# Optimization experiments

Measured on AMD Instinct MI355X. Metric: run time of the kernel, lower is better.

Reference implementation:

```python
import jax, jax.numpy as jnp
import numpy as np

N_NODES = 100000
N_EDGES = 1600000
D_IN = 128
HID = 128
N_CLS = 10
N_GRAPHS = 128


def _gcn_conv(x, W, b, src, dst, dis, n):
    # x' = W x; out[i] = sum_{(j->i)} d_j^{-1/2} d_i^{-1/2} x'_j ; then + bias
    h = x @ W  # [N, out]
    norm = dis[src] * dis[dst]  # [E_tot]
    msg = h[src] * norm[:, None]  # gather + scale (irregular access)
    out = jax.ops.segment_sum(msg, dst, num_segments=n)  # scatter-add
    return out + b


def setup_inputs() -> dict:
    key = jax.random.key(0)
    ks = jax.random.split(key, 12)
    x = jax.random.normal(ks[0], (N_NODES, D_IN), dtype=jnp.float32)
    edge_index = jax.random.randint(ks[1], (2, N_EDGES), 0, N_NODES, dtype=jnp.int64)
    batch = jnp.sort(jax.random.randint(ks[2], (N_NODES,), 0, N_GRAPHS, dtype=jnp.int64))
    drop_u = jax.random.uniform(ks[3], (N_NODES, D_IN), dtype=jnp.float32)
    s = lambda k, sh, fan: jax.random.normal(k, sh, dtype=jnp.float32) / np.sqrt(fan)
    return {
        "x": x, "edge_index": edge_index, "batch": batch, "num_graphs": N_GRAPHS,
        "drop_u": drop_u,
        "lin1_w": s(ks[4], (D_IN, D_IN), D_IN), "lin1_b": jnp.zeros((D_IN,), jnp.float32),
        "conv1_w": s(ks[5], (D_IN, HID), D_IN), "conv1_b": jnp.zeros((HID,), jnp.float32),
        "conv2_w": s(ks[6], (HID, HID // 2), HID), "conv2_b": jnp.zeros((HID // 2,), jnp.float32),
        "lin2_w": s(ks[7], (HID // 2, N_CLS), HID // 2), "lin2_b": jnp.zeros((N_CLS,), jnp.float32),
    }


def reference(x, edge_index, batch, num_graphs, drop_u,
              lin1_w, lin1_b, conv1_w, conv1_b, conv2_w, conv2_b, lin2_w, lin2_b):
    n = x.shape[0]
    # add self loops (PyG GCNConv default)
    loop = jnp.arange(n, dtype=edge_index.dtype)
    src = jnp.concatenate([edge_index[0], loop])
    dst = jnp.concatenate([edge_index[1], loop])
    deg = jax.ops.segment_sum(jnp.ones_like(dst, dtype=x.dtype), dst, num_segments=n)
    dis = jnp.where(deg > 0, jax.lax.rsqrt(deg), 0.0)  # deg^{-1/2}

    h = x @ lin1_w + lin1_b
    h = _gcn_conv(h, conv1_w, conv1_b, src, dst, dis, n)
    # dropout p=0.5 (training mode in original): keep where u >= 0.5, scale by 2
    h = h * (drop_u >= 0.5).astype(h.dtype) * 2.0
    h = jax.nn.relu(h)
    h = _gcn_conv(h, conv2_w, conv2_b, src, dst, dis, n)
    # global mean pool over graph ids
    sums = jax.ops.segment_sum(h, batch, num_segments=num_graphs)
    cnts = jax.ops.segment_sum(jnp.ones((n,), h.dtype), batch, num_segments=num_graphs)
    pooled = sums / jnp.maximum(cnts, 1.0)[:, None]
    return pooled @ lin2_w + lin2_b
```

## Files before the change

### kernel.cpp

```cpp
#include <hip/hip_runtime.h>
#include <hip/hip_bf16.h>

#define DIN   128
#define HID2  64
#define NCLS  10
#define NGRAPH 128
#define SCAN_CHUNK 1024
#define NBLK 256
#define NBKT_MAX 512
#define CAP 6144

typedef __attribute__((ext_vector_type(8))) short bf16x8;
typedef __attribute__((ext_vector_type(4))) float f32x4;

__device__ __forceinline__ void atomAddF(float* p, float v) {
    unsafeAtomicAdd(p, v);
}

__device__ __forceinline__ unsigned short f2bf(float f) {
    unsigned int u = __float_as_uint(f);
    u += 0x7fffu + ((u >> 16) & 1u);
    return (unsigned short)(u >> 16);
}

__global__ __launch_bounds__(128) void k_w12(const float* __restrict__ lw,
                                             const float* __restrict__ lb,
                                             const float* __restrict__ cw,
                                             float* __restrict__ W12,
                                             float* __restrict__ c1preb) {
    int i = blockIdx.x, j = threadIdx.x;
    const float* arow = (i < 128) ? (lw + i * 128) : lb;
    float acc = 0.f;
#pragma unroll 8
    for (int k = 0; k < 128; ++k) acc += arow[k] * cw[k * 128 + j];
    if (i < 128) W12[i * 128 + j] = acc;
    else         c1preb[j] = acc;
}

__global__ __launch_bounds__(256) void k_bhist(const int* __restrict__ dst,
                                               int* __restrict__ bh, int E, int nbkt,
                                               float* __restrict__ zbuf, int zn) {
    __shared__ int lh[NBKT_MAX];
    if (blockIdx.x == 0)
        for (int i = threadIdx.x; i < zn; i += 256) zbuf[i] = 0.f;
    for (int i = threadIdx.x; i < nbkt; i += 256) lh[i] = 0;
    __syncthreads();
    for (int e = blockIdx.x * 256 + threadIdx.x; e < E; e += NBLK * 256)
        atomicAdd(&lh[__builtin_nontemporal_load(dst + e) >> 8], 1);
    __syncthreads();
    for (int i = threadIdx.x; i < nbkt; i += 256) bh[i * NBLK + blockIdx.x] = lh[i];
}

__global__ __launch_bounds__(256) void k_scan_part(const int* __restrict__ cnt,
                                                   int* __restrict__ part, int n) {
    int base = blockIdx.x * SCAN_CHUNK + threadIdx.x * 4;
    int s = 0;
#pragma unroll
    for (int j = 0; j < 4; ++j) { int i = base + j; if (i < n) s += cnt[i]; }
#pragma unroll
    for (int o = 32; o > 0; o >>= 1) s += __shfl_down(s, o);
    __shared__ int wsum[4];
    if ((threadIdx.x & 63) == 0) wsum[threadIdx.x >> 6] = s;
    __syncthreads();
    if (threadIdx.x == 0) part[blockIdx.x] = wsum[0] + wsum[1] + wsum[2] + wsum[3];
}
__global__ __launch_bounds__(256) void k_scan_mid(int* __restrict__ part,
                                                  int* __restrict__ total_out,
                                                  int B, int n) {
    __shared__ int sh[256];
    int t = threadIdx.x;
    int v = (t < B) ? part[t] : 0;
    sh[t] = v;
    __syncthreads();
    for (int off = 1; off < 256; off <<= 1) {
        int u = (t >= off) ? sh[t - off] : 0;
        __syncthreads();
        sh[t] += u;
        __syncthreads();
    }
    if (t < B) part[t] = sh[t] - v;
    if (t == 255) total_out[n] = sh[255];
}
__global__ __launch_bounds__(256) void k_scan_fin2(const int* cnt,
                                                   const int* __restrict__ part,
                                                   int* out, int n) {
    __shared__ int sh[256];
    int t = threadIdx.x;
    int base = blockIdx.x * SCAN_CHUNK + t * 4;
    int c[4]; int s = 0;
#pragma unroll
    for (int j = 0; j < 4; ++j) { int i = base + j; c[j] = (i < n) ? cnt[i] : 0; s += c[j]; }
    sh[t] = s;
    __syncthreads();
    for (int off = 1; off < 256; off <<= 1) {
        int u = (t >= off) ? sh[t - off] : 0;
        __syncthreads();
        sh[t] += u;
        __syncthreads();
    }
    int excl = part[blockIdx.x] + sh[t] - s;
#pragma unroll
    for (int j = 0; j < 4; ++j) {
        int i = base + j;
        if (i < n) out[i] = excl;
        excl += c[j];
    }
}

__global__ __launch_bounds__(256) void k_partition(const int* __restrict__ src,
                                                   const int* __restrict__ dst,
                                                   const int* __restrict__ bh,
                                                   int* __restrict__ pairs, int E, int nbkt) {
    __shared__ int cur[NBKT_MAX];
    for (int i = threadIdx.x; i < nbkt; i += 256) cur[i] = bh[i * NBLK + blockIdx.x];
    __syncthreads();
    for (int e = blockIdx.x * 256 + threadIdx.x; e < E; e += NBLK * 256) {
        int d = __builtin_nontemporal_load(dst + e);
        int s = __builtin_nontemporal_load(src + e);
        int pos = atomicAdd(&cur[d >> 8], 1);
        pairs[pos] = (s << 8) | (d & 255);
    }
}

__global__ __launch_bounds__(256) void k_csr_local(const int* __restrict__ pairs,
                                                   const int* __restrict__ bh,
                                                   int* __restrict__ row_start,
                                                   float* __restrict__ dis,
                                                   int* __restrict__ col,
                                                   int N) {
    __shared__ int cntL[256], scanL[256], curL[256];
    __shared__ int srcbuf[CAP];
    const int tid = threadIdx.x;
    const int lo = blockIdx.x << 8;
    const int bstart = bh[blockIdx.x * NBLK];
    const int bend = bh[(blockIdx.x + 1) * NBLK];
    const int nE = bend - bstart;

    cntL[tid] = 0;
    __syncthreads();
    for (int e = bstart + tid; e < bend; e += 256)
        atomicAdd(&cntL[pairs[e] & 255], 1);
    __syncthreads();
    const int deg = cntL[tid];
    scanL[tid] = deg;
    __syncthreads();
    for (int off = 1; off < 256; off <<= 1) {
        int u = (tid >= off) ? scanL[tid - off] : 0;
        __syncthreads();
        scanL[tid] += u;
        __syncthreads();
    }
    const int excl = scanL[tid] - deg;
    curL[tid] = excl;
    const int node = lo + tid;
    if (node < N) {
        row_start[node] = bstart + excl;
        dis[node] = rsqrtf((float)(deg + 1));
    } else if (node == N) {
        row_start[N] = bend;
    }
    __syncthreads();
    if (nE <= CAP) {
        for (int e = bstart + tid; e < bend; e += 256) {
            int p = pairs[e];
            int pos = atomicAdd(&curL[p & 255], 1);
            srcbuf[pos] = ((unsigned int)p) >> 8;
        }
        __syncthreads();
        for (int i = tid; i < nE; i += 256)
            col[bstart + i] = srcbuf[i];
    } else {
        for (int e = bstart + tid; e < bend; e += 256) {
            int p = pairs[e];
            int pos = atomicAdd(&curL[p & 255], 1);
            col[bstart + pos] = ((unsigned int)p) >> 8;
        }
    }
}

template <int NCOL>
__global__ __launch_bounds__(256) void k_gemm_mfma(const float* __restrict__ A,
                                                   const float* __restrict__ W,
                                                   const float* __restrict__ bias,
                                                   unsigned short* __restrict__ out, int M) {
    constexpr int KP = 136;
    __shared__ unsigned short As[64 * KP];
    __shared__ unsigned short Wt[NCOL * KP];

    const int tid = threadIdx.x;
    const int row0 = blockIdx.x * 64;

    for (int f = tid; f < 2048; f += 256) {
        int r = f >> 5, c4 = f & 31;
        int gr = row0 + r;
        float4 v = make_float4(0.f, 0.f, 0.f, 0.f);
        if (gr < M) v = *(const float4*)(A + (size_t)gr * 128 + c4 * 4);
        ushort4 b;
        b.x = f2bf(v.x); b.y = f2bf(v.y); b.z = f2bf(v.z); b.w = f2bf(v.w);
        *(ushort4*)(&As[r * KP + c4 * 4]) = b;
    }
    for (int f = tid; f < 32 * NCOL; f += 256) {
        int k = f / (NCOL / 4), n4 = f % (NCOL / 4);
        float4 v = *(const float4*)(W + (size_t)k * NCOL + n4 * 4);
        Wt[(n4 * 4 + 0) * KP + k] = f2bf(v.x);
        Wt[(n4 * 4 + 1) * KP + k] = f2bf(v.y);
        Wt[(n4 * 4 + 2) * KP + k] = f2bf(v.z);
        Wt[(n4 * 4 + 3) * KP + k] = f2bf(v.w);
    }
    __syncthreads();

    const int wave = tid >> 6, lane = tid & 63;
    const int quad = lane >> 4, l16 = lane & 15;
    constexpr int CT = (NCOL == 128) ? 2 : 1;
    const int col0 = wave * 16 * CT;

    f32x4 acc[4][CT];
#pragma unroll
    for (int rt = 0; rt < 4; ++rt)
#pragma unroll
        for (int ct = 0; ct < CT; ++ct) acc[rt][ct] = 0.f;

#pragma unroll
    for (int ks = 0; ks < 4; ++ks) {
        const int kbase = ks * 32 + quad * 8;
        bf16x8 bfr[CT];
#pragma unroll
        for (int ct = 0; ct < CT; ++ct)
            bfr[ct] = *(const bf16x8*)(&Wt[(col0 + ct * 16 + l16) * KP + kbase]);
#pragma unroll
        for (int rt = 0; rt < 4; ++rt) {
            bf16x8 afr = *(const bf16x8*)(&As[(rt * 16 + l16) * KP + kbase]);
#pragma unroll
            for (int ct = 0; ct < CT; ++ct)
                acc[rt][ct] = __builtin_amdgcn_mfma_f32_16x16x32_bf16(afr, bfr[ct], acc[rt][ct], 0, 0, 0);
        }
    }

#pragma unroll
    for (int rt = 0; rt < 4; ++rt)
#pragma unroll
        for (int ct = 0; ct < CT; ++ct) {
            const int c = col0 + ct * 16 + l16;
            const float bv = bias ? bias[c] : 0.f;
#pragma unroll
            for (int reg = 0; reg < 4; ++reg) {
                const int gr = row0 + rt * 16 + quad * 4 + reg;
                if (gr < M) out[(size_t)gr * NCOL + c] = f2bf(acc[rt][ct][reg] + bv);
            }
        }
}

__device__ __forceinline__ unsigned int maskbf2(unsigned int w, float ua, float ub) {
    float a = __uint_as_float(w << 16);
    float b = __uint_as_float(w & 0xffff0000u);
    a = (ua >= 0.5f) ? 2.f * fmaxf(a, 0.f) : 0.f;
    b = (ub >= 0.5f) ? 2.f * fmaxf(b, 0.f) : 0.f;
    return (unsigned int)f2bf(a) | ((unsigned int)f2bf(b) << 16);
}

__global__ __launch_bounds__(256) void k_gemm_bf16in(const unsigned short* __restrict__ A,
                                                     const float* __restrict__ W,
                                                     const float* __restrict__ du,
                                                     unsigned short* __restrict__ out, int M) {
    constexpr int NCOL = 64, KP = 136;
    __shared__ unsigned short As[64 * KP];
    __shared__ unsigned short Wt[NCOL * KP];

    const int tid = threadIdx.x;
    const int row0 = blockIdx.x * 64;

    for (int f = tid; f < 1024; f += 256) {
        int r = f >> 4, c8 = f & 15;
        int gr = row0 + r;
        uint4 b = make_uint4(0u, 0u, 0u, 0u);
        if (gr < M) {
            const uint4 v = *(const uint4*)(A + (size_t)gr * 128 + c8 * 8);
            const float4 u0 = *(const float4*)(du + (size_t)gr * 128 + c8 * 8);
            const float4 u1 = *(const float4*)(du + (size_t)gr * 128 + c8 * 8 + 4);
            b.x = maskbf2(v.x, u0.x, u0.y);
            b.y = maskbf2(v.y, u0.z, u0.w);
            b.z = maskbf2(v.z, u1.x, u1.y);
            b.w = maskbf2(v.w, u1.z, u1.w);
        }
        *(uint4*)(&As[r * KP + c8 * 8]) = b;
    }
    for (int f = tid; f < 32 * NCOL; f += 256) {
        int k = f / (NCOL / 4), n4 = f % (NCOL / 4);
        float4 v = *(const float4*)(W + (size_t)k * NCOL + n4 * 4);
        Wt[(n4 * 4 + 0) * KP + k] = f2bf(v.x);
        Wt[(n4 * 4 + 1) * KP + k] = f2bf(v.y);
        Wt[(n4 * 4 + 2) * KP + k] = f2bf(v.z);
        Wt[(n4 * 4 + 3) * KP + k] = f2bf(v.w);
    }
    __syncthreads();

    const int wave = tid >> 6, lane = tid & 63;
    const int quad = lane >> 4, l16 = lane & 15;
    const int col0 = wave * 16;

    f32x4 acc[4];
#pragma unroll
    for (int rt = 0; rt < 4; ++rt) acc[rt] = 0.f;

#pragma unroll
    for (int ks = 0; ks < 4; ++ks) {
        const int kbase = ks * 32 + quad * 8;
        bf16x8 bfr = *(const bf16x8*)(&Wt[(col0 + l16) * KP + kbase]);
#pragma unroll
        for (int rt = 0; rt < 4; ++rt) {
            bf16x8 afr = *(const bf16x8*)(&As[(rt * 16 + l16) * KP + kbase]);
            acc[rt] = __builtin_amdgcn_mfma_f32_16x16x32_bf16(afr, bfr, acc[rt], 0, 0, 0);
        }
    }

#pragma unroll
    for (int rt = 0; rt < 4; ++rt) {
        const int c = col0 + l16;
#pragma unroll
        for (int reg = 0; reg < 4; ++reg) {
            const int gr = row0 + rt * 16 + quad * 4 + reg;
            if (gr < M) out[(size_t)gr * NCOL + c] = f2bf(acc[rt][reg]);
        }
    }
}

__device__ __forceinline__ void bfacc(uint4 v, float d, float* acc) {
    acc[0] = fmaf(d, __uint_as_float(v.x << 16),        acc[0]);
    acc[1] = fmaf(d, __uint_as_float(v.x & 0xffff0000u), acc[1]);
    acc[2] = fmaf(d, __uint_as_float(v.y << 16),        acc[2]);
    acc[3] = fmaf(d, __uint_as_float(v.y & 0xffff0000u), acc[3]);
    acc[4] = fmaf(d, __uint_as_float(v.z << 16),        acc[4]);
    acc[5] = fmaf(d, __uint_as_float(v.z & 0xffff0000u), acc[5]);
    acc[6] = fmaf(d, __uint_as_float(v.w << 16),        acc[6]);
    acc[7] = fmaf(d, __uint_as_float(v.w & 0xffff0000u), acc[7]);
}

__global__ __launch_bounds__(256) void k_gather_h1(const unsigned short* __restrict__ h,
                                                   const int* __restrict__ row_start,
                                                   const int* __restrict__ col,
                                                   const float* __restrict__ dis,
                                                   const float* __restrict__ bias,
                                                   unsigned short* __restrict__ outb, int n) {
    const int node = (blockIdx.x * 256 + (int)threadIdx.x) >> 4;
    const int l = threadIdx.x & 15;
    if (node >= n) return;
    const int coff = l * 8;

    const float dn = dis[node];
    float acc[8];
    {
        uint4 v = *(const uint4*)(h + (size_t)node * 128 + coff);
#pragma unroll
        for (int q = 0; q < 8; ++q) acc[q] = 0.f;
        bfacc(v, dn, acc);
    }

    const int beg = row_start[node], end = row_start[node + 1];
    int j = beg;
    for (; j + 3 < end; j += 4) {
        const int s0 = col[j], s1 = col[j + 1], s2 = col[j + 2], s3 = col[j + 3];
        const float d0 = dis[s0], d1 = dis[s1], d2 = dis[s2], d3 = dis[s3];
        const uint4 v0 = *(const uint4*)(h + (size_t)s0 * 128 + coff);
        const uint4 v1 = *(const uint4*)(h + (size_t)s1 * 128 + coff);
        const uint4 v2 = *(const uint4*)(h + (size_t)s2 * 128 + coff);
        const uint4 v3 = *(const uint4*)(h + (size_t)s3 * 128 + coff);
        bfacc(v0, d0, acc);
        bfacc(v1, d1, acc);
        bfacc(v2, d2, acc);
        bfacc(v3, d3, acc);
    }
    for (; j < end; ++j) {
        const int s0 = col[j];
        const float d0 = dis[s0];
        const uint4 v0 = *(const uint4*)(h + (size_t)s0 * 128 + coff);
        bfacc(v0, d0, acc);
    }

    const float4 b0 = *(const float4*)(bias + coff);
    const float4 b1 = *(const float4*)(bias + coff + 4);
    const float r0 = fmaf(dn, acc[0], b0.x), r1 = fmaf(dn, acc[1], b0.y);
    const float r2 = fmaf(dn, acc[2], b0.z), r3 = fmaf(dn, acc[3], b0.w);
    const float r4 = fmaf(dn, acc[4], b1.x), r5 = fmaf(dn, acc[5], b1.y);
    const float r6 = fmaf(dn, acc[6], b1.z), r7 = fmaf(dn, acc[7], b1.w);
    uint4 o;
    o.x = (unsigned int)f2bf(r0) | ((unsigned int)f2bf(r1) << 16);
    o.y = (unsigned int)f2bf(r2) | ((unsigned int)f2bf(r3) << 16);
    o.z = (unsigned int)f2bf(r4) | ((unsigned int)f2bf(r5) << 16);
    o.w = (unsigned int)f2bf(r6) | ((unsigned int)f2bf(r7) << 16);
    *(uint4*)(outb + (size_t)node * 128 + coff) = o;
}

__global__ __launch_bounds__(256) void k_gather_pool(const unsigned short* __restrict__ h,
                                                     const int* __restrict__ row_start,
                                                     const int* __restrict__ col,
                                                     const float* __restrict__ dis,
                                                     const float* __restrict__ bias,
                                                     const int* __restrict__ batch,
                                                     float* __restrict__ sums,
                                                     float* __restrict__ cnt, int n) {
    const int node = (blockIdx.x * 256 + (int)threadIdx.x) >> 3;
    const int l = threadIdx.x & 7;
    const int coff = l * 8;
    const bool valid = node < n;

    float r[8];
    int g = 0;
    if (valid) {
        const float dn = dis[node];
        g = batch[node];
        float acc[8];
        {
            uint4 v = *(const uint4*)(h + (size_t)node * 64 + coff);
#pragma unroll
            for (int q = 0; q < 8; ++q) acc[q] = 0.f;
            bfacc(v, dn, acc);
        }
        const int beg = row_start[node], end = row_start[node + 1];
        int j = beg;
        for (; j + 3 < end; j += 4) {
            const int s0 = col[j], s1 = col[j + 1], s2 = col[j + 2], s3 = col[j + 3];
            const float d0 = dis[s0], d1 = dis[s1], d2 = dis[s2], d3 = dis[s3];
            const uint4 v0 = *(const uint4*)(h + (size_t)s0 * 64 + coff);
            const uint4 v1 = *(const uint4*)(h + (size_t)s1 * 64 + coff);
            const uint4 v2 = *(const uint4*)(h + (size_t)s2 * 64 + coff);
            const uint4 v3 = *(const uint4*)(h + (size_t)s3 * 64 + coff);
            bfacc(v0, d0, acc);
            bfacc(v1, d1, acc);
            bfacc(v2, d2, acc);
            bfacc(v3, d3, acc);
        }
        for (; j < end; ++j) {
            const int s0 = col[j];
            const float d0 = dis[s0];
            const uint4 v0 = *(const uint4*)(h + (size_t)s0 * 64 + coff);
            bfacc(v0, d0, acc);
        }
        const float4 b0 = *(const float4*)(bias + coff);
        const float4 b1 = *(const float4*)(bias + coff + 4);
        r[0] = fmaf(dn, acc[0], b0.x); r[1] = fmaf(dn, acc[1], b0.y);
        r[2] = fmaf(dn, acc[2], b0.z); r[3] = fmaf(dn, acc[3], b0.w);
        r[4] = fmaf(dn, acc[4], b1.x); r[5] = fmaf(dn, acc[5], b1.y);
        r[6] = fmaf(dn, acc[6], b1.z); r[7] = fmaf(dn, acc[7], b1.w);
    } else {
#pragma unroll
        for (int q = 0; q < 8; ++q) r[q] = 0.f;
    }

    const int g0 = __shfl(g, 0);
    const bool uni = __all(valid && (g == g0));
    if (uni) {
#pragma unroll
        for (int q = 0; q < 8; ++q) {
            r[q] += __shfl_xor(r[q], 8);
            r[q] += __shfl_xor(r[q], 16);
            r[q] += __shfl_xor(r[q], 32);
        }
        const int lane = threadIdx.x & 63;
        if (lane < 8) {
#pragma unroll
            for (int q = 0; q < 8; ++q) atomAddF(&sums[g0 * 64 + lane * 8 + q], r[q]);
            if (lane == 0) atomAddF(&cnt[g0], 8.0f);
        }
    } else if (valid) {
#pragma unroll
        for (int q = 0; q < 8; ++q) atomAddF(&sums[g * 64 + coff + q], r[q]);
        if (l == 0) atomAddF(&cnt[g], 1.0f);
    }
}

__global__ __launch_bounds__(64) void k_final(const float* __restrict__ sums,
                                              const float* __restrict__ cnt,
                                              const float* __restrict__ w,
                                              const float* __restrict__ b,
                                              float* __restrict__ out) {
    int g = blockIdx.x, f = threadIdx.x;
    float c = fmaxf(cnt[g], 1.0f);
    float p = sums[g * 64 + f] / c;
#pragma unroll
    for (int cls = 0; cls < NCLS; ++cls) {
        float v = p * w[f * 10 + cls];
#pragma unroll
        for (int o = 32; o > 0; o >>= 1) v += __shfl_down(v, o);
        if (f == 0) out[g * 10 + cls] = v + b[cls];
    }
}

extern "C" void kernel_launch(void* const* d_in, const int* in_sizes, int n_in,
                              void* d_out, int out_size, void* d_ws, size_t ws_size,
                              hipStream_t stream) {
    const float* x       = (const float*)d_in[0];
    const int*   ei      = (const int*)d_in[1];
    const int*   batch   = (const int*)d_in[2];
    const float* drop_u  = (const float*)d_in[4];
    const float* lin1_w  = (const float*)d_in[5];
    const float* lin1_b  = (const float*)d_in[6];
    const float* conv1_w = (const float*)d_in[7];
    const float* conv1_b = (const float*)d_in[8];
    const float* conv2_w = (const float*)d_in[9];
    const float* conv2_b = (const float*)d_in[10];
    const float* lin2_w  = (const float*)d_in[11];
    const float* lin2_b  = (const float*)d_in[12];
    float* out = (float*)d_out;

    const int N = in_sizes[0] / DIN;
    const int E = in_sizes[1] / 2;
    const int* src = ei;
    const int* dst = ei + E;

    const int nbkt = (N + 255) >> 8;
    const int M = nbkt * NBLK;

    float* ws    = (float*)d_ws;
    float* out1  = ws;
    unsigned short* h1b = (unsigned short*)(ws + (size_t)N * 128);
    float* dis   = ws + (size_t)N * 128 + (size_t)N * 64;
    float* W12   = dis + N;
    float* c1pb  = W12 + 16384;
    float* sums  = c1pb + 128;
    float* cntp  = sums + NGRAPH * 64;
    int*   row_start = (int*)(cntp + NGRAPH);
    int*   part  = row_start + N + 2;
    int*   bh    = part + 256;
    int*   col   = bh + NBKT_MAX * NBLK + 2;
    int*   pairs = col + E;
    unsigned short* h1agg = (unsigned short*)out1;
    unsigned short* h2b = h1b;

    k_w12<<<129, 128, 0, stream>>>(lin1_w, lin1_b, conv1_w, W12, c1pb);

    k_bhist<<<NBLK, 256, 0, stream>>>(dst, bh, E, nbkt, sums, NGRAPH * 64 + NGRAPH);
    const int scanB = (M + SCAN_CHUNK - 1) / SCAN_CHUNK;
    k_scan_part<<<scanB, 256, 0, stream>>>(bh, part, M);
    k_scan_mid<<<1, 256, 0, stream>>>(part, bh, scanB, M);
    k_scan_fin2<<<scanB, 256, 0, stream>>>(bh, part, bh, M);
    k_partition<<<NBLK, 256, 0, stream>>>(src, dst, bh, pairs, E, nbkt);
    k_csr_local<<<nbkt, 256, 0, stream>>>(pairs, bh, row_start, dis, col, N);

    const int gemmGrid = (N + 63) / 64;
    k_gemm_mfma<128><<<gemmGrid, 256, 0, stream>>>(x, W12, c1pb, h1b, N);

    k_gather_h1<<<((size_t)N * 16 + 255) / 256, 256, 0, stream>>>(h1b, row_start, col, dis, conv1_b, h1agg, N);

    k_gemm_bf16in<<<gemmGrid, 256, 0, stream>>>(h1agg, conv2_w, drop_u, h2b, N);

    k_gather_pool<<<((size_t)N * 8 + 255) / 256, 256, 0, stream>>>(h2b, row_start, col, dis, conv2_b, batch, sums, cntp, N);

    k_final<<<NGRAPH, 64, 0, stream>>>(sums, cntp, lin2_w, lin2_b, out);
}
```

Baseline: 421.3 us.

## Replace per-wave pool atomics with block partials and segmented second-pass reduction

The gather-pool kernel now reduces each block's 32 nodes in shared memory when they all belong to one graph. It writes a per-block partial sum, graph id and node count instead of issuing global float atomics from every wave. A new small kernel walks the block partials in contiguous ranges, merging runs with the same graph id before making one atomic per run. Mixed-graph blocks keep the old atomic path. The change adds two block barriers, a shared-memory atomic and an extra kernel launch in exchange for far fewer contended global atomics on the 128 graph rows.

New measurement: 386.6 us. 8.2% less time.

```diff
diff --git a/kernel.cpp b/kernel.cpp
--- a/kernel.cpp
+++ b/kernel.cpp
@@ -396,15 +396,26 @@
                                                      const float* __restrict__ dis,
                                                      const float* __restrict__ bias,
                                                      const int* __restrict__ batch,
+                                                     float* __restrict__ partial,
+                                                     int* __restrict__ bgid,
+                                                     int* __restrict__ bvcnt,
                                                      float* __restrict__ sums,
                                                      float* __restrict__ cnt, int n) {
-    const int node = (blockIdx.x * 256 + (int)threadIdx.x) >> 3;
-    const int l = threadIdx.x & 7;
+    __shared__ float bsum[4][64];
+    __shared__ int sh_gfirst, sh_uni;
+    const int tid = threadIdx.x;
+    const int node = (blockIdx.x * 256 + tid) >> 3;
+    const int l = tid & 7;
     const int coff = l * 8;
     const bool valid = node < n;
+    const int node0 = blockIdx.x * 32;
+
+    if (tid == 0) { sh_gfirst = batch[node0]; sh_uni = 1; }
+    __syncthreads();
+    const int gfirst = sh_gfirst;
 
     float r[8];
-    int g = 0;
+    int g = gfirst;
     if (valid) {
         const float dn = dis[node];
         g = batch[node];
@@ -446,25 +457,85 @@
         for (int q = 0; q < 8; ++q) r[q] = 0.f;
     }
 
-    const int g0 = __shfl(g, 0);
-    const bool uni = __all(valid && (g == g0));
-    if (uni) {
+    if (valid && g != gfirst) atomicAnd(&sh_uni, 0);
+    __syncthreads();
+
+    if (sh_uni) {
 #pragma unroll
         for (int q = 0; q < 8; ++q) {
             r[q] += __shfl_xor(r[q], 8);
             r[q] += __shfl_xor(r[q], 16);
             r[q] += __shfl_xor(r[q], 32);
         }
-        const int lane = threadIdx.x & 63;
+        const int wave = tid >> 6, lane = tid & 63;
         if (lane < 8) {
 #pragma unroll
-            for (int q = 0; q < 8; ++q) atomAddF(&sums[g0 * 64 + lane * 8 + q], r[q]);
-            if (lane == 0) atomAddF(&cnt[g0], 8.0f);
-        }
-    } else if (valid) {
-#pragma unroll
-        for (int q = 0; q < 8; ++q) atomAddF(&sums[g * 64 + coff + q], r[q]);
-        if (l == 0) atomAddF(&cnt[g], 1.0f);
+            for (int q = 0; q < 8; ++q) bsum[wave][lane * 8 + q] = r[q];
+        }
+        __syncthreads();
+        if (tid < 64)
+            partial[(size_t)blockIdx.x * 64 + tid] =
+                bsum[0][tid] + bsum[1][tid] + bsum[2][tid] + bsum[3][tid];
+        if (tid == 0) {
+            bgid[blockIdx.x] = gfirst;
+            bvcnt[blockIdx.x] = min(n - node0, 32);
+        }
+    } else {
+        if (tid == 0) bgid[blockIdx.x] = -1;
+        const int g0 = __shfl(g, 0);
+        const bool wuni = __all(valid && (g == g0));
+        if (wuni) {
+#pragma unroll
+            for (int q = 0; q < 8; ++q) {
+                r[q] += __shfl_xor(r[q], 8);
+                r[q] += __shfl_xor(r[q], 16);
+                r[q] += __shfl_xor(r[q], 32);
+            }
+            const int lane = tid & 63;
+            if (lane < 8) {
+#pragma unroll
+                for (int q = 0; q < 8; ++q) atomAddF(&sums[g0 * 64 + lane * 8 + q], r[q]);
+                if (lane == 0) atomAddF(&cnt[g0], 8.0f);
+            }
+        } else if (valid) {
+#pragma unroll
+            for (int q = 0; q < 8; ++q) atomAddF(&sums[g * 64 + coff + q], r[q]);
+            if (l == 0) atomAddF(&cnt[g], 1.0f);
+        }
+    }
+}
+
+__global__ __launch_bounds__(256) void k_pool2(const float* __restrict__ partial,
+                                               const int* __restrict__ bgid,
+                                               const int* __restrict__ bvcnt,
+                                               float* __restrict__ sums,
+                                               float* __restrict__ cnt, int nb) {
+    const int grp = (blockIdx.x * 256 + (int)threadIdx.x) >> 6;
+    const int f = threadIdx.x & 63;
+    const int ngroups = gridDim.x * 4;
+    const int per = (nb + ngroups - 1) / ngroups;
+    const int start = grp * per, end = min(nb, start + per);
+    if (start >= end) return;
+    int cg = -1;
+    float acc = 0.f;
+    int vc = 0;
+    for (int b = start; b < end; ++b) {
+        const int g = bgid[b];
+        if (g != cg) {
+            if (cg >= 0) {
+                atomAddF(&sums[cg * 64 + f], acc);
+                if (f == 0) atomAddF(&cnt[cg], (float)vc);
+            }
+            acc = 0.f; vc = 0; cg = g;
+        }
+        if (g >= 0) {
+            acc += partial[(size_t)b * 64 + f];
+            vc += bvcnt[b];
+        }
+    }
+    if (cg >= 0) {
+        atomAddF(&sums[cg * 64 + f], acc);
+        if (f == 0) atomAddF(&cnt[cg], (float)vc);
     }
 }
 
@@ -509,6 +580,7 @@
 
     const int nbkt = (N + 255) >> 8;
     const int M = nbkt * NBLK;
+    const int nbGP = (int)(((size_t)N * 8 + 255) / 256);
 
     float* ws    = (float*)d_ws;
     float* out1  = ws;
@@ -523,6 +595,9 @@
     int*   bh    = part + 256;
     int*   col   = bh + NBKT_MAX * NBLK + 2;
     int*   pairs = col + E;
+    float* partial = (float*)(pairs + E);
+    int*   bgid  = (int*)(partial + (size_t)nbGP * 64);
+    int*   bvcnt = bgid + nbGP;
     unsigned short* h1agg = (unsigned short*)out1;
     unsigned short* h2b = h1b;
 
@@ -543,7 +618,9 @@
 
     k_gemm_bf16in<<<gemmGrid, 256, 0, stream>>>(h1agg, conv2_w, drop_u, h2b, N);
 
-    k_gather_pool<<<((size_t)N * 8 + 255) / 256, 256, 0, stream>>>(h2b, row_start, col, dis, conv2_b, batch, sums, cntp, N);
+    k_gather_pool<<<nbGP, 256, 0, stream>>>(h2b, row_start, col, dis, conv2_b, batch,
+                                            partial, bgid, bvcnt, sums, cntp, N);
+    k_pool2<<<16, 256, 0, stream>>>(partial, bgid, bvcnt, sums, cntp, nbGP);
 
     k_final<<<NGRAPH, 64, 0, stream>>>(sums, cntp, lin2_w, lin2_b, out);
 }
```
